# Kernel tuning notes

Hardware: AMD Instinct MI355X
Metric: run time of the kernel (lower is better)

The kernel has to match this reference:

```python
import jax, jax.numpy as jnp
import numpy as np

N_NODES, N_EDGES, IN_DIM, HID, N_FEAT_CLOSE, N_GRAPHS = 100000, 1600000, 128, 64, 5, 512


def _glorot(k, shape):
    lim = float(np.sqrt(6.0 / (shape[0] + shape[1])))
    return jax.random.uniform(k, shape, jnp.float32, -lim, lim)


def setup_inputs() -> dict:
    key = jax.random.key(0)
    ks = jax.random.split(key, 16)
    x = jax.random.normal(ks[0], (N_NODES, IN_DIM), jnp.float32)
    edge_index = jax.random.randint(ks[1], (2, N_EDGES), 0, N_NODES, jnp.int32)
    closeness = jax.random.uniform(ks[2], (N_NODES, N_FEAT_CLOSE), jnp.float32)
    batch = jnp.sort(jax.random.randint(ks[3], (N_NODES,), 0, N_GRAPHS, jnp.int32))
    return {
        'x': x, 'edge_index': edge_index, 'closeness': closeness, 'batch': batch,
        'num_graphs': N_GRAPHS,
        'W1': _glorot(ks[4], (IN_DIM, HID)), 'b1': jnp.zeros((HID,), jnp.float32),
        'W2': _glorot(ks[5], (HID, HID)), 'b2': jnp.zeros((HID,), jnp.float32),
        'W3': _glorot(ks[6], (HID, HID)), 'b3': jnp.zeros((HID,), jnp.float32),
        'Wc': _glorot(ks[7], (N_FEAT_CLOSE, 1)), 'bc': jnp.zeros((1,), jnp.float32),
        'Wa1': _glorot(ks[8], (HID, 16)), 'ba1': jnp.zeros((16,), jnp.float32),
        'Wa2': _glorot(ks[9], (16, 1)), 'ba2': jnp.zeros((1,), jnp.float32),
    }


def reference(x, edge_index, closeness, batch, num_graphs, W1, b1, W2, b2, W3, b3, Wc, bc, Wa1, ba1, Wa2, ba2):
    src, dst = edge_index[0], edge_index[1]
    N = x.shape[0]
    # GCN symmetric normalization with implicit self-loops (weight 1)
    deg = jax.ops.segment_sum(jnp.ones(src.shape, x.dtype), dst, num_segments=N) + 1.0
    dinv = jax.lax.rsqrt(deg)
    norm = dinv[src] * dinv[dst]  # [E]
    self_norm = (dinv * dinv)[:, None]  # 1/deg, self-loop coefficient

    def gcn(h, W, b):
        h = h @ W  # [N, hid]
        agg = jax.ops.segment_sum(h[src] * norm[:, None], dst, num_segments=N)
        return jax.nn.relu(agg + h * self_norm + b)

    h = gcn(x, W1, b1)
    h = gcn(h, W2, b2)
    h = gcn(h, W3, b3)

    # per-graph softmax over closeness scores, scaled by graph size
    s = closeness @ Wc + bc  # [N,1]
    smax = jax.ops.segment_max(s, batch, num_segments=num_graphs)
    e = jnp.exp(s - smax[batch])
    ssum = jax.ops.segment_sum(e, batch, num_segments=num_graphs)
    counts = jax.ops.segment_sum(jnp.ones((N,), x.dtype), batch, num_segments=num_graphs)
    w = (e / ssum[batch]) * counts[batch][:, None]  # [N,1]

    # weighted per-graph max pooling, then tiny MLP per graph
    pooled = jax.ops.segment_max(w * h, batch, num_segments=num_graphs)  # [G,64]
    a = jax.nn.relu(pooled @ Wa1 + ba1)
    return a @ Wa2 + ba2  # [G,1]
```

## Files before the change

kernel.cpp:

```cpp
#include <hip/hip_runtime.h>

#define N_NODESC 100000
#define N_EDGESC 1600000
#define IN_DIMC 128
#define HIDC 64
#define N_GRAPHSC 512
#define PAD_DEG 64


__global__ void zero_bounds_kernel(int* __restrict__ cntR, const int* __restrict__ batch,
                                   int* __restrict__ gstart) {
  int i = blockIdx.x * blockDim.x + threadIdx.x;
  if (i >= N_NODESC) return;
  cntR[i] = 0;
  cntR[N_NODESC + i] = 0;
  cntR[2 * N_NODESC + i] = 0;
  cntR[3 * N_NODESC + i] = 0;
  int b = batch[i];
  int prev = (i == 0) ? -1 : batch[i - 1];
  for (int g = prev + 1; g <= b; ++g) gstart[g] = i;
  if (i == N_NODESC - 1)
    for (int g = b + 1; g <= N_GRAPHSC; ++g) gstart[g] = N_NODESC;
}

__global__ void deg_kernel(const int* __restrict__ dstv, int* __restrict__ cntR,
                           int* __restrict__ slot) {
  int e4 = (blockIdx.x * blockDim.x + threadIdx.x) * 4;
  if (e4 >= N_EDGESC) return;
  int4 d = *(const int4*)(dstv + e4);
  int4 s;
  s.x = atomicAdd(&cntR[d.x], 1);
  s.y = atomicAdd(&cntR[N_NODESC + d.y], 1);
  s.z = atomicAdd(&cntR[2 * N_NODESC + d.z], 1);
  s.w = atomicAdd(&cntR[3 * N_NODESC + d.w], 1);
  *(int4*)(slot + e4) = s;
}

__global__ void off_dinv_kernel(const int* __restrict__ cntR, int* __restrict__ offR,
                                int* __restrict__ cnt, float* __restrict__ dinv) {
  int i = blockIdx.x * blockDim.x + threadIdx.x;
  if (i >= N_NODESC) return;
  int c0 = cntR[i];
  int c1 = cntR[N_NODESC + i];
  int c2 = cntR[2 * N_NODESC + i];
  int c3 = cntR[3 * N_NODESC + i];
  offR[i] = c0;
  offR[N_NODESC + i] = c0 + c1;
  offR[2 * N_NODESC + i] = c0 + c1 + c2;
  int tot = c0 + c1 + c2 + c3;
  cnt[i] = tot;
  dinv[i] = rsqrtf((float)tot + 1.0f);
}

__global__ void fill_pad_kernel(const int* __restrict__ srcv, const int* __restrict__ dstv,
                                const int* __restrict__ slot, const int* __restrict__ offR,
                                int* __restrict__ csr_pad) {
  int e4 = (blockIdx.x * blockDim.x + threadIdx.x) * 4;
  if (e4 >= N_EDGESC) return;
  int4 s = *(const int4*)(srcv + e4);
  int4 d = *(const int4*)(dstv + e4);
  int4 sl = *(const int4*)(slot + e4);
  int p0 = sl.x;
  int p1 = offR[d.y] + sl.y;
  int p2 = offR[N_NODESC + d.z] + sl.z;
  int p3 = offR[2 * N_NODESC + d.w] + sl.w;
  if (p0 < PAD_DEG) __builtin_nontemporal_store(s.x, &csr_pad[d.x * PAD_DEG + p0]);
  if (p1 < PAD_DEG) __builtin_nontemporal_store(s.y, &csr_pad[d.y * PAD_DEG + p1]);
  if (p2 < PAD_DEG) __builtin_nontemporal_store(s.z, &csr_pad[d.z * PAD_DEG + p2]);
  if (p3 < PAD_DEG) __builtin_nontemporal_store(s.w, &csr_pad[d.w * PAD_DEG + p3]);
}


#define GT_M 128
#define XS_LD 132
template <int KT>
__global__ void __launch_bounds__(256, 3)
gemm_tile_kernel(const float* __restrict__ X, const float* __restrict__ W,
                 const float* __restrict__ dinv, float* __restrict__ T) {
  __shared__ float xs[64 * XS_LD];
  __shared__ float ws[64 * 64];
  int t = threadIdx.x;
  int base = blockIdx.x * GT_M;
  int r0 = (t >> 4) * 8;
  int c0 = (t & 15) * 4;
  float acc[8][4];
#pragma unroll
  for (int i = 0; i < 8; ++i)
#pragma unroll
    for (int j = 0; j < 4; ++j) acc[i][j] = 0.f;

  int kq = (t & 15) * 4;
  int rr = t >> 4;

  for (int kb = 0; kb < KT; kb += 64) {
    if (kb) __syncthreads();
#pragma unroll
    for (int it = 0; it < 8; ++it) {
      int r = rr + it * 16;
      int grow = base + r;
      if (grow >= N_NODESC) grow = N_NODESC - 1;
      float4 q = *(const float4*)(X + (size_t)grow * KT + kb + kq);
      xs[(kq + 0) * XS_LD + r] = q.x;
      xs[(kq + 1) * XS_LD + r] = q.y;
      xs[(kq + 2) * XS_LD + r] = q.z;
      xs[(kq + 3) * XS_LD + r] = q.w;
    }
#pragma unroll
    for (int it = 0; it < 4; ++it) {
      int idx = (it * 256 + t) * 4;
      *(float4*)(ws + idx) = *(const float4*)(W + (size_t)kb * HIDC + idx);
    }
    __syncthreads();
#pragma unroll 8
    for (int k = 0; k < 64; ++k) {
      float4 xa = *(const float4*)(xs + k * XS_LD + r0);
      float4 xb = *(const float4*)(xs + k * XS_LD + r0 + 4);
      float4 wf = *(const float4*)(ws + k * 64 + c0);
      float xf[8] = {xa.x, xa.y, xa.z, xa.w, xb.x, xb.y, xb.z, xb.w};
      float wv[4] = {wf.x, wf.y, wf.z, wf.w};
#pragma unroll
      for (int i = 0; i < 8; ++i)
#pragma unroll
        for (int j = 0; j < 4; ++j) acc[i][j] = fmaf(xf[i], wv[j], acc[i][j]);
    }
  }
#pragma unroll
  for (int i = 0; i < 8; ++i) {
    int row = base + r0 + i;
    if (row < N_NODESC) {
      float dv = dinv[row];
      float4 o;
      o.x = acc[i][0] * dv;
      o.y = acc[i][1] * dv;
      o.z = acc[i][2] * dv;
      o.w = acc[i][3] * dv;
      *(float4*)(T + (size_t)row * HIDC + c0) = o;
    }
  }
}

__global__ void gather_kernel(const float* __restrict__ ts, const float* __restrict__ dinv,
                              const int* __restrict__ cnt, const int* __restrict__ csr_pad,
                              const float* __restrict__ bias, float* __restrict__ h) {
  int lane = threadIdx.x & 63;
  int node = (blockIdx.x * blockDim.x + threadIdx.x) >> 6;
  if (node >= N_NODESC) return;
  int deg = min(cnt[node], PAD_DEG);
  const int* __restrict__ row = csr_pad + node * PAD_DEG;
  float sum = ts[node * HIDC + lane];
  int e = 0;
  for (; e + 16 <= deg; e += 16) {
    int si[16];
#pragma unroll
    for (int j = 0; j < 16; ++j) si[j] = row[e + j];
    float v[16];
#pragma unroll
    for (int j = 0; j < 16; ++j) v[j] = ts[si[j] * HIDC + lane];
    float s0 = ((v[0] + v[1]) + (v[2] + v[3])) + ((v[4] + v[5]) + (v[6] + v[7]));
    float s1 = ((v[8] + v[9]) + (v[10] + v[11])) + ((v[12] + v[13]) + (v[14] + v[15]));
    sum += s0 + s1;
  }
  for (; e + 8 <= deg; e += 8) {
    int s0 = row[e], s1 = row[e + 1], s2 = row[e + 2], s3 = row[e + 3];
    int s4 = row[e + 4], s5 = row[e + 5], s6 = row[e + 6], s7 = row[e + 7];
    float v0 = ts[s0 * HIDC + lane];
    float v1 = ts[s1 * HIDC + lane];
    float v2 = ts[s2 * HIDC + lane];
    float v3 = ts[s3 * HIDC + lane];
    float v4 = ts[s4 * HIDC + lane];
    float v5 = ts[s5 * HIDC + lane];
    float v6 = ts[s6 * HIDC + lane];
    float v7 = ts[s7 * HIDC + lane];
    sum += ((v0 + v1) + (v2 + v3)) + ((v4 + v5) + (v6 + v7));
  }
  for (; e + 4 <= deg; e += 4) {
    int s0 = row[e], s1 = row[e + 1], s2 = row[e + 2], s3 = row[e + 3];
    float v0 = ts[s0 * HIDC + lane];
    float v1 = ts[s1 * HIDC + lane];
    float v2 = ts[s2 * HIDC + lane];
    float v3 = ts[s3 * HIDC + lane];
    sum += (v0 + v1) + (v2 + v3);
  }
  for (; e < deg; ++e) sum += ts[row[e] * HIDC + lane];
  h[node * HIDC + lane] = fmaxf(sum * dinv[node] + bias[lane], 0.f);
}

__global__ void __launch_bounds__(256)
readout_kernel(const float* __restrict__ h, const float* __restrict__ closeness,
               const float* __restrict__ Wc, const float* __restrict__ bc,
               const int* __restrict__ gstart, const float* __restrict__ Wa1,
               const float* __restrict__ ba1, const float* __restrict__ Wa2,
               const float* __restrict__ ba2, float* __restrict__ out) {
  __shared__ float sArr[1024];
  __shared__ float red[256];
  __shared__ float cross[4 * 64];
  int g = blockIdx.x;
  int t = threadIdx.x;
  int n0 = gstart[g], n1 = gstart[g + 1];
  int count = n1 - n0;
  int cap = min(count, 1024);
  float wc0 = Wc[0], wc1 = Wc[1], wc2 = Wc[2], wc3 = Wc[3], wc4 = Wc[4], bcv = bc[0];
  float lmax = -3.4e38f;
  for (int idx = t; idx < cap; idx += 256) {
    const float* c = closeness + (size_t)(n0 + idx) * 5;
    float s = fmaf(c[4], wc4, fmaf(c[3], wc3, fmaf(c[2], wc2, fmaf(c[1], wc1, fmaf(c[0], wc0, bcv)))));
    sArr[idx] = s;
    lmax = fmaxf(lmax, s);
  }
  red[t] = lmax;
  __syncthreads();
  for (int s = 128; s > 0; s >>= 1) {
    if (t < s) red[t] = fmaxf(red[t], red[t + s]);
    __syncthreads();
  }
  float m = red[0];
  __syncthreads();
  float lsum = 0.f;
  for (int idx = t; idx < cap; idx += 256) {
    float e = expf(sArr[idx] - m);
    sArr[idx] = e;
    lsum += e;
  }
  red[t] = lsum;
  __syncthreads();
  for (int s = 128; s > 0; s >>= 1) {
    if (t < s) red[t] += red[t + s];
    __syncthreads();
  }
  float scale = (count > 0) ? ((float)count / red[0]) : 0.f;
  __syncthreads();
  int wv = t >> 6, lane = t & 63;
  float pmax = 0.f;
  for (int idx = wv; idx < cap; idx += 4) {
    float w = sArr[idx] * scale;
    pmax = fmaxf(pmax, w * h[(size_t)(n0 + idx) * HIDC + lane]);
  }
  cross[wv * 64 + lane] = pmax;
  __syncthreads();
  if (wv == 0) {
    float p = fmaxf(fmaxf(cross[lane], cross[64 + lane]),
                    fmaxf(cross[128 + lane], cross[192 + lane]));
    float o = 0.f;
#pragma unroll
    for (int tt = 0; tt < 16; ++tt) {
      float prod = p * Wa1[lane * 16 + tt];
#pragma unroll
      for (int off = 32; off > 0; off >>= 1) prod += __shfl_xor(prod, off);
      float a = fmaxf(prod + ba1[tt], 0.f);
      o += a * Wa2[tt];
    }
    if (lane == 0) out[g] = o + ba2[0];
  }
}


extern "C" void kernel_launch(void* const* d_in, const int* in_sizes, int n_in,
                              void* d_out, int out_size, void* d_ws, size_t ws_size,
                              hipStream_t stream) {
  const float* x = (const float*)d_in[0];
  const int* ei = (const int*)d_in[1];
  const float* closeness = (const float*)d_in[2];
  const int* batch = (const int*)d_in[3];
  const float* W1 = (const float*)d_in[5];
  const float* b1 = (const float*)d_in[6];
  const float* W2 = (const float*)d_in[7];
  const float* b2 = (const float*)d_in[8];
  const float* W3 = (const float*)d_in[9];
  const float* b3 = (const float*)d_in[10];
  const float* Wc = (const float*)d_in[11];
  const float* bc = (const float*)d_in[12];
  const float* Wa1 = (const float*)d_in[13];
  const float* ba1 = (const float*)d_in[14];
  const float* Wa2 = (const float*)d_in[15];
  const float* ba2 = (const float*)d_in[16];
  float* out = (float*)d_out;
  const int* srcv = ei;
  const int* dstv = ei + N_EDGESC;

  char* ws = (char*)d_ws;
  size_t off = 0;
  auto alloc = [&](size_t bytes) -> void* {
    void* p = ws + off;
    off = (off + bytes + 255) & ~(size_t)255;
    return p;
  };
  float* tbuf = (float*)alloc(sizeof(float) * N_NODESC * HIDC);
  float* hbuf = (float*)alloc(sizeof(float) * N_NODESC * HIDC);
  int* csr_pad = (int*)alloc(sizeof(int) * N_NODESC * PAD_DEG);
  int* slot = (int*)alloc(sizeof(int) * N_EDGESC);
  int* cntR = (int*)alloc(sizeof(int) * N_NODESC * 4);
  int* offR = (int*)alloc(sizeof(int) * N_NODESC * 3);
  int* cnt = (int*)alloc(sizeof(int) * N_NODESC);
  float* dinv = (float*)alloc(sizeof(float) * N_NODESC);
  int* gstart = (int*)alloc(sizeof(int) * (N_GRAPHSC + 1));

  const int B = 256;
  int gN = (N_NODESC + B - 1) / B;
  int gE4 = (N_EDGESC / 4 + B - 1) / B;
  int gGather = (N_NODESC * 64) / B;
  int gTile = (N_NODESC + GT_M - 1) / GT_M;

  zero_bounds_kernel<<<gN, B, 0, stream>>>(cntR, batch, gstart);
  deg_kernel<<<gE4, B, 0, stream>>>(dstv, cntR, slot);
  off_dinv_kernel<<<gN, B, 0, stream>>>(cntR, offR, cnt, dinv);
  fill_pad_kernel<<<gE4, B, 0, stream>>>(srcv, dstv, slot, offR, csr_pad);

  gemm_tile_kernel<IN_DIMC><<<gTile, B, 0, stream>>>(x, W1, dinv, tbuf);
  gather_kernel<<<gGather, B, 0, stream>>>(tbuf, dinv, cnt, csr_pad, b1, hbuf);
  gemm_tile_kernel<HIDC><<<gTile, B, 0, stream>>>(hbuf, W2, dinv, tbuf);
  gather_kernel<<<gGather, B, 0, stream>>>(tbuf, dinv, cnt, csr_pad, b2, hbuf);
  gemm_tile_kernel<HIDC><<<gTile, B, 0, stream>>>(hbuf, W3, dinv, tbuf);
  gather_kernel<<<gGather, B, 0, stream>>>(tbuf, dinv, cnt, csr_pad, b3, hbuf);

  readout_kernel<<<N_GRAPHSC, B, 0, stream>>>(hbuf, closeness, Wc, bc, gstart,
                                              Wa1, ba1, Wa2, ba2, out);
}
```

Measured before the change: 517.7 us.

## Fuse degree counting into first GEMM launch and defer source normalization to gather

The layer-1 GEMM no longer needs dinv, so it now runs in the same launch as the edge degree atomics, as extra blocks of one grid. The source-side dinv scaling moves into the first gather, which multiplies each neighbour value by dinv[src]. This removes the serialization between degree computation and the largest GEMM and drops a launch. In exchange, the first gather does an extra random dinv load per edge. The 8-wide gather remainder loop is also removed.

```diff
diff --git a/kernel.cpp b/kernel.cpp
--- a/kernel.cpp
+++ b/kernel.cpp
@@ -21,19 +21,6 @@
   for (int g = prev + 1; g <= b; ++g) gstart[g] = i;
   if (i == N_NODESC - 1)
     for (int g = b + 1; g <= N_GRAPHSC; ++g) gstart[g] = N_NODESC;
-}
-
-__global__ void deg_kernel(const int* __restrict__ dstv, int* __restrict__ cntR,
-                           int* __restrict__ slot) {
-  int e4 = (blockIdx.x * blockDim.x + threadIdx.x) * 4;
-  if (e4 >= N_EDGESC) return;
-  int4 d = *(const int4*)(dstv + e4);
-  int4 s;
-  s.x = atomicAdd(&cntR[d.x], 1);
-  s.y = atomicAdd(&cntR[N_NODESC + d.y], 1);
-  s.z = atomicAdd(&cntR[2 * N_NODESC + d.z], 1);
-  s.w = atomicAdd(&cntR[3 * N_NODESC + d.w], 1);
-  *(int4*)(slot + e4) = s;
 }
 
 __global__ void off_dinv_kernel(const int* __restrict__ cntR, int* __restrict__ offR,
@@ -73,14 +60,16 @@
 
 #define GT_M 128
 #define XS_LD 132
-template <int KT>
-__global__ void __launch_bounds__(256, 3)
-gemm_tile_kernel(const float* __restrict__ X, const float* __restrict__ W,
-                 const float* __restrict__ dinv, float* __restrict__ T) {
-  __shared__ float xs[64 * XS_LD];
-  __shared__ float ws[64 * 64];
+#define GT_BLOCKS ((N_NODESC + GT_M - 1) / GT_M)
+
+template <int KT, bool APPLY_DINV>
+__device__ __forceinline__ void gemm_tile_body(const float* __restrict__ X,
+                                               const float* __restrict__ W,
+                                               const float* __restrict__ dinv,
+                                               float* __restrict__ T, int blk,
+                                               float* __restrict__ xs, float* __restrict__ ws) {
   int t = threadIdx.x;
-  int base = blockIdx.x * GT_M;
+  int base = blk * GT_M;
   int r0 = (t >> 4) * 8;
   int c0 = (t & 15) * 4;
   float acc[8][4];
@@ -128,7 +117,7 @@
   for (int i = 0; i < 8; ++i) {
     int row = base + r0 + i;
     if (row < N_NODESC) {
-      float dv = dinv[row];
+      float dv = APPLY_DINV ? dinv[row] : 1.0f;
       float4 o;
       o.x = acc[i][0] * dv;
       o.y = acc[i][1] * dv;
@@ -139,6 +128,38 @@
   }
 }
 
+template <int KT, bool APPLY_DINV>
+__global__ void __launch_bounds__(256, 3)
+gemm_tile_kernel(const float* __restrict__ X, const float* __restrict__ W,
+                 const float* __restrict__ dinv, float* __restrict__ T) {
+  __shared__ float xs[64 * XS_LD];
+  __shared__ float ws[64 * 64];
+  gemm_tile_body<KT, APPLY_DINV>(X, W, dinv, T, blockIdx.x, xs, ws);
+}
+
+template <int KT>
+__global__ void __launch_bounds__(256, 3)
+gemm1_deg_kernel(const float* __restrict__ X, const float* __restrict__ W,
+                 float* __restrict__ T, const int* __restrict__ dstv,
+                 int* __restrict__ cntR, int* __restrict__ slot) {
+  __shared__ float xs[64 * XS_LD];
+  __shared__ float ws[64 * 64];
+  if (blockIdx.x < GT_BLOCKS) {
+    gemm_tile_body<KT, false>(X, W, nullptr, T, blockIdx.x, xs, ws);
+  } else {
+    int e4 = ((blockIdx.x - GT_BLOCKS) * blockDim.x + threadIdx.x) * 4;
+    if (e4 >= N_EDGESC) return;
+    int4 d = *(const int4*)(dstv + e4);
+    int4 s;
+    s.x = atomicAdd(&cntR[d.x], 1);
+    s.y = atomicAdd(&cntR[N_NODESC + d.y], 1);
+    s.z = atomicAdd(&cntR[2 * N_NODESC + d.z], 1);
+    s.w = atomicAdd(&cntR[3 * N_NODESC + d.w], 1);
+    *(int4*)(slot + e4) = s;
+  }
+}
+
+template <bool SCALE_SRC>
 __global__ void gather_kernel(const float* __restrict__ ts, const float* __restrict__ dinv,
                               const int* __restrict__ cnt, const int* __restrict__ csr_pad,
                               const float* __restrict__ bias, float* __restrict__ h) {
@@ -147,31 +168,34 @@
   if (node >= N_NODESC) return;
   int deg = min(cnt[node], PAD_DEG);
   const int* __restrict__ row = csr_pad + node * PAD_DEG;
-  float sum = ts[node * HIDC + lane];
+  float dvn = dinv[node];
+  float self = ts[node * HIDC + lane];
+  float sum = SCALE_SRC ? self * dvn : self;
   int e = 0;
   for (; e + 16 <= deg; e += 16) {
     int si[16];
 #pragma unroll
     for (int j = 0; j < 16; ++j) si[j] = row[e + j];
+    float dv[16];
+    if (SCALE_SRC) {
+#pragma unroll
+      for (int j = 0; j < 16; ++j) dv[j] = dinv[si[j]];
+    }
     float v[16];
 #pragma unroll
     for (int j = 0; j < 16; ++j) v[j] = ts[si[j] * HIDC + lane];
-    float s0 = ((v[0] + v[1]) + (v[2] + v[3])) + ((v[4] + v[5]) + (v[6] + v[7]));
-    float s1 = ((v[8] + v[9]) + (v[10] + v[11])) + ((v[12] + v[13]) + (v[14] + v[15]));
-    sum += s0 + s1;
-  }
-  for (; e + 8 <= deg; e += 8) {
-    int s0 = row[e], s1 = row[e + 1], s2 = row[e + 2], s3 = row[e + 3];
-    int s4 = row[e + 4], s5 = row[e + 5], s6 = row[e + 6], s7 = row[e + 7];
-    float v0 = ts[s0 * HIDC + lane];
-    float v1 = ts[s1 * HIDC + lane];
-    float v2 = ts[s2 * HIDC + lane];
-    float v3 = ts[s3 * HIDC + lane];
-    float v4 = ts[s4 * HIDC + lane];
-    float v5 = ts[s5 * HIDC + lane];
-    float v6 = ts[s6 * HIDC + lane];
-    float v7 = ts[s7 * HIDC + lane];
-    sum += ((v0 + v1) + (v2 + v3)) + ((v4 + v5) + (v6 + v7));
+    if (SCALE_SRC) {
+      float s0 = 0.f, s1 = 0.f;
+#pragma unroll
+      for (int j = 0; j < 8; ++j) s0 = fmaf(v[j], dv[j], s0);
+#pragma unroll
+      for (int j = 8; j < 16; ++j) s1 = fmaf(v[j], dv[j], s1);
+      sum += s0 + s1;
+    } else {
+      float s0 = ((v[0] + v[1]) + (v[2] + v[3])) + ((v[4] + v[5]) + (v[6] + v[7]));
+      float s1 = ((v[8] + v[9]) + (v[10] + v[11])) + ((v[12] + v[13]) + (v[14] + v[15]));
+      sum += s0 + s1;
+    }
   }
   for (; e + 4 <= deg; e += 4) {
     int s0 = row[e], s1 = row[e + 1], s2 = row[e + 2], s3 = row[e + 3];
@@ -179,10 +203,19 @@
     float v1 = ts[s1 * HIDC + lane];
     float v2 = ts[s2 * HIDC + lane];
     float v3 = ts[s3 * HIDC + lane];
-    sum += (v0 + v1) + (v2 + v3);
-  }
-  for (; e < deg; ++e) sum += ts[row[e] * HIDC + lane];
-  h[node * HIDC + lane] = fmaxf(sum * dinv[node] + bias[lane], 0.f);
+    if (SCALE_SRC) {
+      float a = fmaf(v0, dinv[s0], v1 * dinv[s1]);
+      float b = fmaf(v2, dinv[s2], v3 * dinv[s3]);
+      sum += a + b;
+    } else {
+      sum += (v0 + v1) + (v2 + v3);
+    }
+  }
+  for (; e < deg; ++e) {
+    float v = ts[row[e] * HIDC + lane];
+    sum += SCALE_SRC ? v * dinv[row[e]] : v;
+  }
+  h[node * HIDC + lane] = fmaxf(sum * dvn + bias[lane], 0.f);
 }
 
 __global__ void __launch_bounds__(256)
@@ -298,19 +331,17 @@
   int gN = (N_NODESC + B - 1) / B;
   int gE4 = (N_EDGESC / 4 + B - 1) / B;
   int gGather = (N_NODESC * 64) / B;
-  int gTile = (N_NODESC + GT_M - 1) / GT_M;
 
   zero_bounds_kernel<<<gN, B, 0, stream>>>(cntR, batch, gstart);
-  deg_kernel<<<gE4, B, 0, stream>>>(dstv, cntR, slot);
+  gemm1_deg_kernel<IN_DIMC><<<GT_BLOCKS + gE4, B, 0, stream>>>(x, W1, tbuf, dstv, cntR, slot);
   off_dinv_kernel<<<gN, B, 0, stream>>>(cntR, offR, cnt, dinv);
   fill_pad_kernel<<<gE4, B, 0, stream>>>(srcv, dstv, slot, offR, csr_pad);
 
-  gemm_tile_kernel<IN_DIMC><<<gTile, B, 0, stream>>>(x, W1, dinv, tbuf);
-  gather_kernel<<<gGather, B, 0, stream>>>(tbuf, dinv, cnt, csr_pad, b1, hbuf);
-  gemm_tile_kernel<HIDC><<<gTile, B, 0, stream>>>(hbuf, W2, dinv, tbuf);
-  gather_kernel<<<gGather, B, 0, stream>>>(tbuf, dinv, cnt, csr_pad, b2, hbuf);
-  gemm_tile_kernel<HIDC><<<gTile, B, 0, stream>>>(hbuf, W3, dinv, tbuf);
-  gather_kernel<<<gGather, B, 0, stream>>>(tbuf, dinv, cnt, csr_pad, b3, hbuf);
+  gather_kernel<true><<<gGather, B, 0, stream>>>(tbuf, dinv, cnt, csr_pad, b1, hbuf);
+  gemm_tile_kernel<HIDC, true><<<GT_BLOCKS, B, 0, stream>>>(hbuf, W2, dinv, tbuf);
+  gather_kernel<false><<<gGather, B, 0, stream>>>(tbuf, dinv, cnt, csr_pad, b2, hbuf);
+  gemm_tile_kernel<HIDC, true><<<GT_BLOCKS, B, 0, stream>>>(hbuf, W3, dinv, tbuf);
+  gather_kernel<false><<<gGather, B, 0, stream>>>(tbuf, dinv, cnt, csr_pad, b3, hbuf);
 
   readout_kernel<<<N_GRAPHSC, B, 0, stream>>>(hbuf, closeness, Wc, bc, gstart,
                                               Wa1, ba1, Wa2, ba2, out);
```

Result: slower. 541.6 us (+4.6%).
